# Kernel optimization log

Hardware: AMD Instinct MI355X
Metric: run time of the kernel (lower is better)

## Reference

```python
import jax, jax.numpy as jnp
import numpy as np
from math import factorial, sqrt, pi

# ---- sizes ----
LMAX = 2; K = 32; NL = 4; NB = 8; PPOLY = 5.0; RMAX = 10.0
N = 1000; E = 8000; G = 4; XDIM = 26; MLP = 128
LS = (0, 1, 2)

# ---- real Clebsch-Gordan couplings (Racah formula + complex->real basis change) ----
def _cg_c(j1, m1, j2, m2, J, M):
    if M != m1 + m2 or J < abs(j1 - j2) or J > j1 + j2:
        return 0.0
    f = factorial
    pre = sqrt((2*J+1) * f(J+j1-j2) * f(J-j1+j2) * f(j1+j2-J) / f(j1+j2+J+1))
    pre *= sqrt(f(J+M)*f(J-M)*f(j1-m1)*f(j1+m1)*f(j2-m2)*f(j2+m2))
    s = 0.0
    for k in range(j1 + j2 - J + 1):
        d = (k, j1+j2-J-k, j1-m1-k, j2+m2-k, J-j2+m1+k, J-j1-m2+k)
        if min(d) < 0:
            continue
        den = 1.0
        for t in d:
            den *= f(t)
        s += (-1.0)**k / den
    return pre * s

def _u(l):
    U = np.zeros((2*l+1, 2*l+1), dtype=complex)
    for m in range(-l, l+1):
        i = m + l
        if m < 0:
            U[i, m+l] = 1j/sqrt(2); U[i, -m+l] = -1j*((-1.0)**m)/sqrt(2)
        elif m == 0:
            U[i, l] = 1.0
        else:
            U[i, -m+l] = 1/sqrt(2); U[i, m+l] = ((-1.0)**m)/sqrt(2)
    return U

def _real_cg(l1, l2, l3):
    Tc = np.zeros((2*l1+1, 2*l2+1, 2*l3+1), dtype=complex)
    for m1 in range(-l1, l1+1):
        for m2 in range(-l2, l2+1):
            Tc[m1+l1, m2+l2, :] = [_cg_c(l1, m1, l2, m2, l3, m3) for m3 in range(-l3, l3+1)]
    T = np.einsum('am,bn,co,mno->abc', _u(l1), _u(l2), _u(l3).conj(), Tc)
    T = T.real if np.abs(T.real).sum() >= np.abs(T.imag).sum() else T.imag
    return jnp.asarray(np.ascontiguousarray(T), dtype=jnp.float32)

CG = {}
for _l1 in LS:
    for _l2 in LS:
        for _l3 in LS:
            if abs(_l1-_l2) <= _l3 <= _l1+_l2 and (_l1+_l2+_l3) % 2 == 0:
                CG[(_l1, _l2, _l3)] = _real_cg(_l1, _l2, _l3)

CONVH = sorted(CG.keys())                 # 11 parity-allowed (l_in, l_sh, l_out) paths
CONV0 = [p for p in CONVH if p[0] == 0]   # 3 paths for first layer (Kx0e input)
NUMEL0 = len(CONV0) * K * K
NUMELH = len(CONVH) * K * K

PAIRS = {lo: [(l1, l2) for l1 in LS for l2 in LS if (l1, l2, lo) in CG] for lo in LS}
TRIPLES = {lo: [(l1, l2, L, l3) for L in LS for l3 in LS if (L, l3, lo) in CG
                for (l1, l2) in PAIRS[L]] for lo in LS}
MAXP2 = max(len(PAIRS[lo]) for lo in LS)     # 4
MAXP3 = max(len(TRIPLES[lo]) for lo in LS)   # 15
CG3 = {}
for _lo in LS:
    for (_a, _b, _L, _c) in TRIPLES[_lo]:
        CG3[(_a, _b, _L, _c, _lo)] = jnp.einsum('ijl,lmo->ijmo', CG[(_a, _b, _L)], CG[(_L, _c, _lo)])

# ---- geometry embeddings ----
def _sph(u):  # u: [E,3] unit vectors; component-normalized real SH, l=0..2
    x, y, z = u[:, 0], u[:, 1], u[:, 2]
    y0 = jnp.ones_like(x)[:, None]
    y1 = sqrt(3.0) * jnp.stack([y, z, x], -1)
    y2 = jnp.stack([sqrt(15.0)*x*y, sqrt(15.0)*y*z, sqrt(5.0)/2*(3*z*z - 1),
                    sqrt(15.0)*x*z, sqrt(15.0)/2*(x*x - y*y)], -1)
    return (y0, y1, y2)

def _radial(r):  # r: [E,1] -> [E,NB] Bessel basis * polynomial cutoff (p=5)
    n = jnp.arange(1, NB + 1, dtype=r.dtype)
    bess = sqrt(2.0 / RMAX) * jnp.sin(n * pi * r / RMAX) / r
    u = r / RMAX
    p = PPOLY
    cut = 1 - (p+1)*(p+2)/2 * u**5 + p*(p+2) * u**6 - p*(p+1)/2 * u**7
    return bess * jnp.where(u < 1.0, cut, 0.0)

# ---- tensor-product conv: per-edge MLP weights -> gather, CG tensor product, scatter-sum ----
def _conv(h, src, dst, sh, ef, w1, b1, w2, b2, paths):
    w = jax.nn.relu(ef @ w1 + b1) @ w2 + b2          # [E, weight_numel]
    nto = {lo: max(1, sum(1 for q in paths if q[2] == lo)) for lo in LS}
    msg = [jnp.zeros((src.shape[0], K, 2*lo + 1), w.dtype) for lo in LS]
    off = 0
    for (li, ls, lo) in paths:
        wp = w[:, off:off + K*K].reshape(-1, K, K); off += K * K
        t = jnp.einsum('eui,es,iso->euo', h[li][src], sh[ls], CG[(li, ls, lo)])
        msg[lo] = msg[lo] + jnp.einsum('euo,euv->evo', t, wp) / sqrt(K * nto[lo])
    return [jnp.zeros((N, K, 2*lo + 1), w.dtype).at[dst].add(msg[lo]) for lo in LS]

def _bn(h, w, b, eps=1e-5):  # e3nn-style irreps batch norm (training stats)
    out = []
    for l in LS:
        xl = h[l]
        if l == 0:
            mu = jnp.mean(xl, axis=0, keepdims=True)
            var = jnp.mean((xl - mu)**2, axis=0, keepdims=True)
            out.append((xl - mu) / jnp.sqrt(var + eps) * w[l][None, :, None] + b[None, :, None])
        else:
            n2 = jnp.mean(jnp.sum(xl * xl, -1), axis=0)  # [K]
            out.append(xl / jnp.sqrt(n2 + eps)[None, :, None] * w[l][None, :, None])
    return out

# ---- equivariant product-basis block (per-channel symmetric contractions, correlation 3) ----
def _prod(A, sc, w1, w2, w3, wlin, target_ls, use_sc):
    out = []
    for lo in target_ls:
        acc = w1[lo][None, :, None] * A[lo]
        for p, (l1, l2) in enumerate(PAIRS[lo]):
            t = jnp.einsum('nki,nkj,ijo->nko', A[l1], A[l2], CG[(l1, l2, lo)])
            acc = acc + w2[lo, p][None, :, None] * t
        for p, (l1, l2, L, l3) in enumerate(TRIPLES[lo]):
            t = jnp.einsum('nki,nkj,nkm,ijmo->nko', A[l1], A[l2], A[l3], CG3[(l1, l2, L, l3, lo)])
            acc = acc + w3[lo, p][None, :, None] * t
        y = jnp.einsum('nki,kv->nvi', acc, wlin[lo])
        if use_sc:
            y = y + sc[lo]
        out.append(y)
    return out

def _forward(x, pos, w_emb, b_emb, fc0_w1, fc0_b1, fc0_w2, fc0_b2,
             fcs_w1, fcs_b1, fcs_w2, fcs_b2, bn_w, bn_b, pw1, pw2, pw3, plin,
             edge_index, batch):
    src, dst = edge_index[0], edge_index[1]
    vec = pos[src] - pos[dst]
    r = jnp.maximum(jnp.linalg.norm(vec, axis=-1, keepdims=True), 1e-6)
    sh = _sph(vec / r)
    ef = _radial(r)
    h0 = x @ w_emb + b_emb
    h = [h0[:, :, None], jnp.zeros((N, K, 3), h0.dtype), jnp.zeros((N, K, 5), h0.dtype)]
    for i in range(NL):
        if i == 0:
            m = _conv(h, src, dst, sh, ef, fc0_w1, fc0_b1, fc0_w2, fc0_b2, CONV0)
        else:
            j = i - 1
            m = _conv(h, src, dst, sh, ef, fcs_w1[j], fcs_b1[j], fcs_w2[j], fcs_b2[j], CONVH)
        m = _bn(m, bn_w[i], bn_b[i])
        last = (i == NL - 1)
        h = _prod(m, h, pw1[i], pw2[i], pw3[i], plin[i],
                  target_ls=((0,) if last else LS), use_sc=(not last))
    node = h[0][:, :, 0]                                  # [N, K]
    graph = jax.ops.segment_sum(node, batch, num_segments=G)
    return node, graph

def setup_inputs() -> dict:
    key = jax.random.key(0)
    ks = jax.random.split(key, 16)
    rn = lambda k, sh, s: jax.random.normal(k, sh, dtype=jnp.float32) * s
    return dict(
        x=rn(ks[0], (N, XDIM), 1.0),
        pos=rn(ks[1], (N, 3), 3.0),
        edge_index=jax.random.randint(ks[2], (2, E), 0, N, dtype=jnp.int32),
        batch=jnp.sort(jax.random.randint(ks[3], (N,), 0, G, dtype=jnp.int32)),
        w_emb=rn(ks[4], (XDIM, K), 1.0/sqrt(XDIM)), b_emb=jnp.zeros((K,), jnp.float32),
        fc0_w1=rn(ks[5], (NB, MLP), 1.0/sqrt(NB)), fc0_b1=jnp.zeros((MLP,), jnp.float32),
        fc0_w2=rn(ks[6], (MLP, NUMEL0), 1.0/sqrt(MLP)), fc0_b2=jnp.zeros((NUMEL0,), jnp.float32),
        fcs_w1=rn(ks[7], (NL-1, NB, MLP), 1.0/sqrt(NB)), fcs_b1=jnp.zeros((NL-1, MLP), jnp.float32),
        fcs_w2=rn(ks[8], (NL-1, MLP, NUMELH), 1.0/sqrt(MLP)), fcs_b2=jnp.zeros((NL-1, NUMELH), jnp.float32),
        bn_w=jnp.ones((NL, 3, K), jnp.float32), bn_b=jnp.zeros((NL, K), jnp.float32),
        pw1=rn(ks[9], (NL, 3, K), 0.5),
        pw2=rn(ks[10], (NL, 3, MAXP2, K), 0.3),
        pw3=rn(ks[11], (NL, 3, MAXP3, K), 0.1),
        plin=rn(ks[12], (NL, 3, K, K), 1.0/sqrt(K)),
    )

def reference(x, pos, edge_index, batch, w_emb, b_emb, fc0_w1, fc0_b1, fc0_w2, fc0_b2,
              fcs_w1, fcs_b1, fcs_w2, fcs_b2, bn_w, bn_b, pw1, pw2, pw3, plin):
    return _forward(x, pos, w_emb, b_emb, fc0_w1, fc0_b1, fc0_w2, fc0_b2,
                    fcs_w1, fcs_b1, fcs_w2, fcs_b2, bn_w, bn_b, pw1, pw2, pw3, plin,
                    edge_index, batch)
```

## Files before the change

kernel.cpp:

```cpp
#include <hip/hip_runtime.h>
#include <hip/hip_bf16.h>
#include <math.h>

#define NE 8000
#define NN 1000
#define CAP 64
#define PLANE 256000

typedef unsigned short ushortt;
typedef __attribute__((ext_vector_type(8))) short short8;
typedef __attribute__((ext_vector_type(4))) float f32x4;

__device__ const int KEYL[11][3] = {{0,0,0},{0,1,1},{0,2,2},{1,0,1},{1,1,0},{1,1,2},{1,2,1},{2,0,2},{2,1,1},{2,2,0},{2,2,2}};
__device__ const int KEYOFF[12] = {0,1,10,35,44,53,98,143,168,213,238,363};

struct PathT { int li, ls, lo, cgoff, comp; };
__device__ const PathT PATHS[11] = {
 {0,0,0,  0, 0},{0,1,1,  1, 1},{0,2,2, 10, 4},{1,0,1, 35, 9},{1,1,0, 44,12},{1,1,2, 53,13},
 {1,2,1, 98,18},{2,0,2,143,21},{2,1,1,168,26},{2,2,0,213,29},{2,2,2,238,30}};

struct CPair { int l1,l2,cga; };
struct CTrip { int l1,l2,L,cga,l3,cgb; };
constexpr CPair cPR0[3]={{0,0,0},{1,1,44},{2,2,213}};
constexpr CPair cPR1[4]={{0,1,1},{1,0,35},{1,2,98},{2,1,168}};
constexpr CPair cPR2[4]={{0,2,10},{1,1,53},{2,0,143},{2,2,238}};
constexpr CTrip cTR0[11]={
  {0,0,0,0,0,0},{1,1,0,44,0,0},{2,2,0,213,0,0},
  {0,1,1,1,1,44},{1,0,1,35,1,44},{1,2,1,98,1,44},{2,1,1,168,1,44},
  {0,2,2,10,2,213},{1,1,2,53,2,213},{2,0,2,143,2,213},{2,2,2,238,2,213}};
constexpr CTrip cTR1[15]={
  {0,0,0,0,1,1},{1,1,0,44,1,1},{2,2,0,213,1,1},
  {0,1,1,1,0,35},{1,0,1,35,0,35},{1,2,1,98,0,35},{2,1,1,168,0,35},
  {0,1,1,1,2,98},{1,0,1,35,2,98},{1,2,1,98,2,98},{2,1,1,168,2,98},
  {0,2,2,10,1,168},{1,1,2,53,1,168},{2,0,2,143,1,168},{2,2,2,238,1,168}};
constexpr CTrip cTR2[15]={
  {0,0,0,0,2,10},{1,1,0,44,2,10},{2,2,0,213,2,10},
  {0,1,1,1,1,53},{1,0,1,35,1,53},{1,2,1,98,1,53},{2,1,1,168,1,53},
  {0,2,2,10,0,143},{1,1,2,53,0,143},{2,0,2,143,0,143},{2,2,2,238,0,143},
  {0,2,2,10,2,238},{1,1,2,53,2,238},{2,0,2,143,2,238},{2,2,2,238,2,238}};
constexpr CPair getPR(int lo,int p){ return lo==0?cPR0[p]:(lo==1?cPR1[p]:cPR2[p]); }
constexpr CTrip getTR(int lo,int p){ return lo==0?cTR0[p]:(lo==1?cTR1[p]:cTR2[p]); }
constexpr int cloff(int l){ return l==0?0:(l==1?1:4); }
constexpr int nPR(int lo){ return lo==0?3:4; }
constexpr int nTR(int lo){ return lo==0?11:15; }

template<int I> struct ic_t { static constexpr int v = I; };
template<int N, int I=0, typename F>
__device__ __forceinline__ void sfor(F&& f){
  if constexpr (I < N){ f(ic_t<I>{}); sfor<N, I+1>((F&&)f); }
}

__device__ __forceinline__ int loff_(int l){ return l==0?0:(l==1?1:4); }

__device__ __forceinline__ ushortt f2bf(float x){
  union { float f; unsigned int u; } a; a.f = x;
  unsigned int r = a.u + 0x7FFFu + ((a.u >> 16) & 1u);
  return (ushortt)(r >> 16);
}

__device__ __forceinline__ void gload_lds16(const void* g, void* lds){
  __builtin_amdgcn_global_load_lds((const __attribute__((address_space(1))) void*)g,
                                   (__attribute__((address_space(3))) void*)lds, 16, 0, 0);
}

__device__ double d_fact(int n){ double f=1.0; for(int i=2;i<=n;i++) f*=(double)i; return f; }

__device__ double d_cg(int j1,int m1,int j2,int m2,int J,int M){
  if (M != m1+m2 || J < abs(j1-j2) || J > j1+j2) return 0.0;
  double pre = sqrt((2.0*J+1.0)*d_fact(J+j1-j2)*d_fact(J-j1+j2)*d_fact(j1+j2-J)/d_fact(j1+j2+J+1));
  pre *= sqrt(d_fact(J+M)*d_fact(J-M)*d_fact(j1-m1)*d_fact(j1+m1)*d_fact(j2-m2)*d_fact(j2+m2));
  double s=0.0;
  for(int k=0;k<=j1+j2-J;k++){
    int d0=k, d1=j1+j2-J-k, d2=j1-m1-k, d3=j2+m2-k, d4=J-j2+m1+k, d5=J-j1-m2+k;
    if (d0<0||d1<0||d2<0||d3<0||d4<0||d5<0) continue;
    double den = d_fact(d0)*d_fact(d1)*d_fact(d2)*d_fact(d3)*d_fact(d4)*d_fact(d5);
    s += ((k&1)?-1.0:1.0)/den;
  }
  return pre*s;
}

__device__ void d_u(int l, int i, int j, double* re, double* im){
  int m = i - l;
  *re=0.0; *im=0.0;
  const double s2 = 0.70710678118654752440;
  double par = (m & 1) ? -1.0 : 1.0;
  if (m < 0){
    if (j == m + l)  *im += s2;
    if (j == -m + l) *im += -par*s2;
  } else if (m == 0){
    if (j == l) *re = 1.0;
  } else {
    if (j == -m + l) *re += s2;
    if (j == m + l)  *re += par*s2;
  }
}

__global__ __launch_bounds__(128) void kcg1(double* tmp){
  int key = blockIdx.x;
  int l1=KEYL[key][0], l2=KEYL[key][1], l3=KEYL[key][2];
  int n1=2*l1+1, n2=2*l2+1, n3=2*l3+1;
  int nel=n1*n2*n3;
  int t=threadIdx.x;
  if (t>=nel) return;
  int a=t/(n2*n3), b=(t/n3)%n2, c=t%n3;
  double sre=0.0, sim=0.0;
  for (int mi=0;mi<n1;mi++)
    for (int ni=0;ni<n2;ni++){
      int m3 = (mi-l1)+(ni-l2);
      int oi = m3 + l3;
      if (oi<0 || oi>=n3) continue;
      double tc = d_cg(l1,mi-l1,l2,ni-l2,l3,m3);
      if (tc==0.0) continue;
      double r1,i1,r2,i2,r3,i3;
      d_u(l1,a,mi,&r1,&i1);
      d_u(l2,b,ni,&r2,&i2);
      d_u(l3,c,oi,&r3,&i3);
      double rr = r1*r2 - i1*i2;
      double ri = r1*i2 + i1*r2;
      double fr = rr*r3 + ri*i3;
      double fi = ri*r3 - rr*i3;
      sre += fr*tc; sim += fi*tc;
    }
  tmp[(size_t)(KEYOFF[key]+t)*2]   = sre;
  tmp[(size_t)(KEYOFF[key]+t)*2+1] = sim;
}

__global__ __launch_bounds__(64) void kcg2(const double* tmp, float* cgf){
  int key=threadIdx.x;
  if (key>=11) return;
  int off=KEYOFF[key], n=KEYOFF[key+1]-off;
  double sre=0.0, sim=0.0;
  for (int i=0;i<n;i++){ sre += fabs(tmp[(size_t)(off+i)*2]); sim += fabs(tmp[(size_t)(off+i)*2+1]); }
  bool takeRe = (sre >= sim);
  for (int i=0;i<n;i++) cgf[off+i] = (float)(takeRe ? tmp[(size_t)(off+i)*2] : tmp[(size_t)(off+i)*2+1]);
}

__global__ __launch_bounds__(256) void kgeom(const float* __restrict__ pos, const int* __restrict__ ei,
                                             float* __restrict__ shb, float* __restrict__ efb){
  int e = blockIdx.x*256+threadIdx.x;
  if (e>=NE) return;
  int s=ei[e], d=ei[NE+e];
  float vx=pos[s*3]-pos[d*3], vy=pos[s*3+1]-pos[d*3+1], vz=pos[s*3+2]-pos[d*3+2];
  float r = sqrtf(vx*vx+vy*vy+vz*vz);
  r = fmaxf(r, 1e-6f);
  float inv = 1.0f/r;
  float x=vx*inv, y=vy*inv, z=vz*inv;
  float* sh = shb + (size_t)e*9;
  const float s3=1.7320508075688772f, s15=3.872983346207417f, s5h=1.118033988749895f, s15h=1.9364916731037085f;
  sh[0]=1.0f;
  sh[1]=s3*y; sh[2]=s3*z; sh[3]=s3*x;
  sh[4]=s15*x*y; sh[5]=s15*y*z; sh[6]=s5h*(3.0f*z*z-1.0f); sh[7]=s15*x*z; sh[8]=s15h*(x*x-y*y);
  float u=r*0.1f;
  float cut=0.0f;
  if (u<1.0f){ float u2=u*u; float u5=u2*u2*u; cut = 1.0f - 21.0f*u5 + 35.0f*u5*u - 15.0f*u5*u2; }
  const float c0 = 0.4472135954999579f;
  const float PIF = 3.14159265358979323846f;
  float* ef = efb + (size_t)e*8;
  for (int j=0;j<8;j++)
    ef[j] = c0*sinf((float)(j+1)*PIF*r*0.1f)*inv*cut;
}

__global__ __launch_bounds__(256) void kembed(const float* __restrict__ x, const float* __restrict__ wemb,
                                              const float* __restrict__ bemb, float* __restrict__ h){
  int idx = blockIdx.x*256+threadIdx.x;
  if (idx>=NN*32) return;
  int n=idx>>5, k=idx&31;
  float a=bemb[k];
  for (int d=0;d<26;d++) a += x[n*26+d]*wemb[d*32+k];
  float* hp = h + (size_t)n*288 + k*9;
  hp[0]=a;
  #pragma unroll
  for (int c=1;c<9;c++) hp[c]=0.0f;
}

__global__ __launch_bounds__(256) void ktrans(const float* __restrict__ fc0_w2, const float* __restrict__ fcs_w2,
                                              ushortt* __restrict__ w2t0, ushortt* __restrict__ w2tH){
  int layer = blockIdx.z;
  int numel = (layer==0) ? 3072 : 11264;
  int c0 = blockIdx.x*32;
  if (c0 >= numel) return;
  const float* src = (layer==0) ? fc0_w2 : fcs_w2 + (size_t)(layer-1)*128*11264;
  ushortt* dst = (layer==0) ? w2t0 : w2tH + (size_t)(layer-1)*11264*128;
  int k0 = blockIdx.y*32;
  __shared__ float tile[32][33];
  int t = threadIdx.x;
  #pragma unroll
  for (int it=0; it<4; it++){
    int r = (t>>5) + it*8;
    tile[r][t&31] = src[(size_t)(k0+r)*numel + c0 + (t&31)];
  }
  __syncthreads();
  #pragma unroll
  for (int it=0; it<4; it++){
    int c = (t>>5) + it*8;
    int k = t&31;
    dst[(size_t)(c0+c)*128 + k0 + k] = f2bf(tile[k][c]);
  }
}

__global__ __launch_bounds__(256) void khid(const float* __restrict__ efb, const float* __restrict__ w1,
                                            const float* __restrict__ b1, ushortt* __restrict__ hidbf){
  int idx = blockIdx.x*256+threadIdx.x;
  if (idx >= NE*128) return;
  int e = idx>>7, m = idx&127;
  float a = b1[m];
  const float* ef = efb + (size_t)e*8;
  #pragma unroll
  for (int j=0;j<8;j++) a = fmaf(ef[j], w1[j*128+m], a);
  a = a>0.0f?a:0.0f;
  hidbf[idx] = f2bf(a);
}

template<int NO>
__global__ __launch_bounds__(256, (NO==1?3:2)) void kmsg5(
    const float* __restrict__ hc, const float* __restrict__ shb,
    const ushortt* __restrict__ hidbf, const ushortt* __restrict__ w2t,
    const float* __restrict__ b2, const float* __restrict__ cg,
    const int* __restrict__ src, float* __restrict__ msgp, int plist){
  int p = (plist >> (blockIdx.y*8)) & 0xFF;
  int e0 = blockIdx.x*64;
  int li=PATHS[p].li, ls=PATHS[p].ls;
  int n1=2*li+1, ns=2*ls+1;
  int lioff=loff_(li), lsoff=loff_(ls);
  int cgoff=PATHS[p].cgoff;
  int comp=PATHS[p].comp;

  __shared__ __align__(16) ushortt sB[2][64*128];
  __shared__ __align__(16) float   sT[NO*2048];
  __shared__ __align__(16) float   sB2[1024];
  __shared__ int     sSRC[64];
  float* ov  = (float*)&sB[1][0];
  float* sCP = ov;
  float* sSH = ov + 1600;

  int t = threadIdx.x;
  int w = t>>6, l = t&63;

  #pragma unroll
  for (int q=0;q<4;q++){
    int R0 = w*16 + q*4;
    int row = R0 + (l>>4);
    int ks = ((l&15)*8) ^ ((row&7)<<3);
    gload_lds16(w2t + (size_t)(p*1024 + row)*128 + ks, &sB[0][R0*128]);
  }
  short8 av[4];
  {
    const ushortt* ap = hidbf + (size_t)(e0 + w*16 + (l&15))*128 + (l>>4)*8;
    #pragma unroll
    for (int kk=0;kk<4;kk++) av[kk] = *(const short8*)(ap + kk*32);
  }
  #pragma unroll
  for (int q=0;q<4;q++) sB2[t + q*256] = b2[p*1024 + t + q*256];
  if (t < 64) sSRC[t] = src[e0+t];
  for (int idx=t; idx<64*9; idx+=256) sSH[idx] = shb[(size_t)e0*9 + idx];
  __syncthreads();

  for (int idx=t; idx<64*n1*NO; idx+=256){
    int e=idx/(n1*NO), r=idx%(n1*NO), i=r/NO, o=r%NO;
    float a=0.0f;
    for (int s=0;s<ns;s++) a += cg[cgoff + (i*ns+s)*NO+o]*sSH[e*9 + lsoff + s];
    sCP[e*25 + i*NO + o]=a;
  }
  __syncthreads();

  for (int idx=t; idx<64*32; idx+=256){
    int e = idx&63, u = idx>>6;
    const float* hp = hc + (size_t)sSRC[e]*288 + u*9 + lioff;
    float hv[5];
    #pragma unroll
    for (int i=0;i<5;i++) hv[i] = hp[i];
    #pragma unroll
    for (int o=0;o<NO;o++){
      float a=0.0f;
      #pragma unroll
      for (int i=0;i<5;i++) if (i<n1) a = fmaf(hv[i], sCP[e*25 + i*NO + o], a);
      sT[(u*NO+o)*64 + e] = a;
    }
  }
  __syncthreads();

  float macc[4][2][NO];
  #pragma unroll
  for (int r=0;r<4;r++)
    #pragma unroll
    for (int vh=0;vh<2;vh++)
      #pragma unroll
      for (int o=0;o<NO;o++) macc[r][vh][o]=0.0f;

  int e_idx = w*16 + (l>>4)*4;

  for (int c=0;c<16;c++){
    int buf = c&1;
    if (c<15){
      #pragma unroll
      for (int q=0;q<4;q++){
        int R0 = w*16 + q*4;
        int row = R0 + (l>>4);
        int ks = ((l&15)*8) ^ ((row&7)<<3);
        gload_lds16(w2t + (size_t)(p*1024 + (c+1)*64 + row)*128 + ks, &sB[buf^1][R0*128]);
      }
    }
    f32x4 acc[4];
    #pragma unroll
    for (int fn=0;fn<4;fn++)
      #pragma unroll
      for (int r=0;r<4;r++) acc[fn][r]=0.0f;
    __builtin_amdgcn_s_setprio(1);
    #pragma unroll
    for (int kk=0; kk<4; kk++){
      #pragma unroll
      for (int fn=0; fn<4; fn++){
        int brow = fn*16 + (l&15);
        int kb = (kk*32 + (l>>4)*8) ^ ((brow&7)<<3);
        short8 bv = *(const short8*)&sB[buf][brow*128 + kb];
        acc[fn] = __builtin_amdgcn_mfma_f32_16x16x32_bf16(av[kk], bv, acc[fn], 0,0,0);
      }
    }
    __builtin_amdgcn_s_setprio(0);
    #pragma unroll
    for (int uu=0;uu<2;uu++){
      int ug = c*2 + uu;
      f32x4 tv[NO];
      #pragma unroll
      for (int o=0;o<NO;o++) tv[o] = *(const f32x4*)&sT[(ug*NO+o)*64 + e_idx];
      #pragma unroll
      for (int vh=0;vh<2;vh++){
        int fn = uu*2+vh;
        float b2v = sB2[c*64 + fn*16 + (l&15)];
        #pragma unroll
        for (int r=0;r<4;r++){
          float Cv = acc[fn][r] + b2v;
          #pragma unroll
          for (int o=0;o<NO;o++) macc[r][vh][o] = fmaf(Cv, tv[o][r], macc[r][vh][o]);
        }
      }
    }
    __syncthreads();
  }

  float* sW = sT;
  #pragma unroll
  for (int r=0;r<4;r++){
    int e = e_idx + r;
    #pragma unroll
    for (int vh=0;vh<2;vh++){
      int v = vh*16 + (l&15);
      int g = v>>2;
      int addr = e*32 + (((g ^ (e&7)))<<2) + (v&3);
      #pragma unroll
      for (int o=0;o<NO;o++)
        sW[o*2048 + addr] = macc[r][vh][o];
    }
  }
  __syncthreads();
  for (int j=t; j<NO*512; j+=256){
    int o = j>>9, q = j&511;
    int e = q>>3, gl = q&7;
    f32x4 vv = *(const f32x4*)&sW[o*2048 + e*32 + ((gl^(e&7))<<2)];
    *(f32x4*)(msgp + (size_t)(comp+o)*PLANE + (size_t)e0*32 + q*4) = vv;
  }
}

__global__ __launch_bounds__(320) void kbuild(const int* __restrict__ dst, int* __restrict__ cnt, int* __restrict__ lst){
  int n = blockIdx.x;
  int t = threadIdx.x;
  __shared__ int s_dstl[NE];
  __shared__ int s_cnt[321];
  for (int idx=t; idx<NE; idx+=320) s_dstl[idx]=dst[idx];
  __syncthreads();
  const int per = NE/320;
  int start=t*per, end=start+per;
  int c=0;
  for (int e=start;e<end;++e) if (s_dstl[e]==n) c++;
  s_cnt[t+1]=c;
  if (t==0) s_cnt[0]=0;
  __syncthreads();
  if (t==0){ for (int i=1;i<=320;i++) s_cnt[i]+=s_cnt[i-1]; }
  __syncthreads();
  int pos = s_cnt[t];
  for (int e=start;e<end;++e) if (s_dstl[e]==n){ if (pos<CAP) lst[n*CAP+pos]=e; pos++; }
  if (t==0){ int M=s_cnt[320]; cnt[n]=(M<CAP)?M:CAP; }
}

__global__ __launch_bounds__(320) void kgather2(const float* __restrict__ msgp, const int* __restrict__ cnt,
                                                const int* __restrict__ lst, float* __restrict__ mbuf, int full){
  int n = blockIdx.x;
  int t = threadIdx.x;
  if (t >= 288) return;
  int M = cnt[n];
  int jc = t>>5, k = t&31;
  float acc=0.0f;
  if (full){
    int pl0,pl1,pl2,pl3,np;
    if (jc==0){ pl0=0; pl1=12; pl2=29; pl3=0; np=3; }
    else if (jc<4){ int o=jc-1; pl0=1+o; pl1=9+o; pl2=18+o; pl3=26+o; np=4; }
    else { int o=jc-4; pl0=4+o; pl1=13+o; pl2=21+o; pl3=30+o; np=4; }
    for (int m=0;m<M;++m){
      int e = lst[n*CAP+m];
      int base = e*32 + k;
      float a = msgp[(size_t)pl0*PLANE + base] + msgp[(size_t)pl1*PLANE + base] + msgp[(size_t)pl2*PLANE + base];
      if (np==4) a += msgp[(size_t)pl3*PLANE + base];
      acc += a;
    }
  } else {
    for (int m=0;m<M;++m){
      int e = lst[n*CAP+m];
      acc += msgp[(size_t)jc*PLANE + e*32 + k];
    }
  }
  float norm = full ? (jc==0 ? 0.10206207261596577f : 0.08838834764831845f) : 0.17677669529663687f;
  mbuf[(size_t)n*288 + k*9 + jc] = acc*norm;
}

__global__ __launch_bounds__(256) void kbn(const float* __restrict__ mbuf, float* __restrict__ stats){
  int k = blockIdx.x, t = threadIdx.x;
  float s0=0,sq0=0,sq1=0,sq2=0;
  for (int n=t;n<NN;n+=256){
    const float* mp = mbuf + (size_t)n*288 + k*9;
    float v0=mp[0]; s0+=v0; sq0+=v0*v0;
    float a=mp[1],b=mp[2],c=mp[3]; sq1+=a*a+b*b+c*c;
    float d=mp[4],e=mp[5],f=mp[6],g=mp[7],h=mp[8]; sq2+=d*d+e*e+f*f+g*g+h*h;
  }
  __shared__ float r[4][256];
  r[0][t]=s0; r[1][t]=sq0; r[2][t]=sq1; r[3][t]=sq2;
  __syncthreads();
  for (int s=128;s>0;s>>=1){
    if (t<s){ r[0][t]+=r[0][t+s]; r[1][t]+=r[1][t+s]; r[2][t]+=r[2][t+s]; r[3][t]+=r[3][t+s]; }
    __syncthreads();
  }
  if (t==0){
    float mu = r[0][0]/(float)NN;
    float var = r[1][0]/(float)NN - mu*mu;
    stats[k]      = mu;
    stats[32+k]   = rsqrtf(var + 1e-5f);
    stats[64+k]   = rsqrtf(r[2][0]/(float)NN + 1e-5f);
    stats[96+k]   = rsqrtf(r[3][0]/(float)NN + 1e-5f);
  }
}

template<int CGA,int NA,int AO,int NB,int BO,int NO>
__device__ __forceinline__ void c2u(const float* __restrict__ cg, const float (&A)[9], const float (&B)[9], float (&out)[5]){
  #pragma unroll
  for (int o=0;o<NO;o++) out[o]=0.0f;
  #pragma unroll
  for (int i=0;i<NA;i++){
    #pragma unroll
    for (int j=0;j<NB;j++){
      float ab=A[AO+i]*B[BO+j];
      #pragma unroll
      for (int o=0;o<NO;o++) out[o]=fmaf(ab, cg[CGA+(i*NB+j)*NO+o], out[o]);
    }
  }
}
template<int CGA,int NA,int NB,int BO,int NO>
__device__ __forceinline__ void c2u5(const float* __restrict__ cg, const float (&Bb)[5], const float (&A)[9], float (&out)[5]){
  #pragma unroll
  for (int o=0;o<NO;o++) out[o]=0.0f;
  #pragma unroll
  for (int i=0;i<NA;i++){
    #pragma unroll
    for (int j=0;j<NB;j++){
      float ab=Bb[i]*A[BO+j];
      #pragma unroll
      for (int o=0;o<NO;o++) out[o]=fmaf(ab, cg[CGA+(i*NB+j)*NO+o], out[o]);
    }
  }
}

template<int LO>
__device__ __forceinline__ void do_lo(const float* __restrict__ cg, const float (&A)[9], float (&L)[9],
                                      const float* __restrict__ w1, const float* __restrict__ w2,
                                      const float* __restrict__ w3, int k){
  constexpr int NO=2*LO+1, AO=cloff(LO);
  float acc[5];
  float wc = w1[LO*32+k];
  #pragma unroll
  for (int o=0;o<NO;o++) acc[o]=wc*A[AO+o];
  sfor<nPR(LO)>([&](auto pc){
    constexpr int p = decltype(pc)::v;
    constexpr CPair P = getPR(LO,p);
    float tt[5];
    c2u<P.cga, 2*P.l1+1, cloff(P.l1), 2*P.l2+1, cloff(P.l2), NO>(cg, A, A, tt);
    float w = w2[(LO*4+p)*32+k];
    #pragma unroll
    for (int o=0;o<NO;o++) acc[o]=fmaf(w, tt[o], acc[o]);
  });
  sfor<nTR(LO)>([&](auto pc){
    constexpr int p = decltype(pc)::v;
    constexpr CTrip T = getTR(LO,p);
    constexpr int NL=2*T.L+1;
    float bb[5];
    c2u<T.cga, 2*T.l1+1, cloff(T.l1), 2*T.l2+1, cloff(T.l2), NL>(cg, A, A, bb);
    float tt[5];
    c2u5<T.cgb, NL, 2*T.l3+1, cloff(T.l3), NO>(cg, bb, A, tt);
    float w = w3[(LO*15+p)*32+k];
    #pragma unroll
    for (int o=0;o<NO;o++) acc[o]=fmaf(w, tt[o], acc[o]);
  });
  #pragma unroll
  for (int o=0;o<NO;o++) L[AO+o]=acc[o];
}

template<int LAST>
__global__ __launch_bounds__(256) void kprod3(const float* __restrict__ mbuf, const float* __restrict__ stats,
    const float* __restrict__ hc, float* __restrict__ hn,
    const float* __restrict__ bnw, const float* __restrict__ bnb,
    const float* __restrict__ w1, const float* __restrict__ w2, const float* __restrict__ w3,
    const float* __restrict__ plin, const float* __restrict__ cg, float* __restrict__ nodeout){
  int t = threadIdx.x;
  int nl = t>>5, k = t&31;
  int n = blockIdx.x*8 + nl;
  __shared__ float sL[8][32][9];
  float A[9], L[9];
  #pragma unroll
  for (int j=0;j<9;j++) L[j]=0.0f;
  const float* mp = mbuf + (size_t)n*288 + k*9;
  {
    float a0 = (mp[0]-stats[k])*stats[32+k]*bnw[k] + bnb[k];
    float f1 = stats[64+k]*bnw[32+k];
    float f2 = stats[96+k]*bnw[64+k];
    A[0]=a0;
    A[1]=mp[1]*f1; A[2]=mp[2]*f1; A[3]=mp[3]*f1;
    #pragma unroll
    for (int c=0;c<5;c++) A[4+c]=mp[4+c]*f2;
  }
  do_lo<0>(cg, A, L, w1, w2, w3, k);
  if constexpr (!LAST){
    do_lo<1>(cg, A, L, w1, w2, w3, k);
    do_lo<2>(cg, A, L, w1, w2, w3, k);
  }
  #pragma unroll
  for (int j=0;j<9;j++) sL[nl][k][j]=L[j];
  __syncthreads();

  if constexpr (!LAST){
    for (int idx=t; idx<8*288; idx+=256){
      int n2 = idx/288;
      int r  = idx%288;
      int jc = r>>5, v = r&31;
      int lo = (jc==0)?0:((jc<4)?1:2);
      float y=0.0f;
      const float* pl = plin + lo*1024 + v;
      for (int kk=0;kk<32;kk++)
        y = fmaf(sL[n2][kk][jc], pl[kk*32], y);
      int ng = blockIdx.x*8 + n2;
      y += hc[(size_t)ng*288 + v*9 + jc];
      hn[(size_t)ng*288 + v*9 + jc] = y;
    }
  } else {
    int n2 = t>>5, v = t&31;
    float y=0.0f;
    const float* pl = plin + v;
    for (int kk=0;kk<32;kk++)
      y = fmaf(sL[n2][kk][0], pl[kk*32], y);
    nodeout[(size_t)(blockIdx.x*8+n2)*32 + v] = y;
  }
}

__global__ __launch_bounds__(256) void kgraphA(const float* __restrict__ nodeout, const int* __restrict__ batch,
                                               float* __restrict__ partial){
  int b = blockIdx.x;
  int t = threadIdx.x;
  __shared__ float sv[8][32];
  __shared__ int   sg[8];
  int nl = t>>5, k = t&31;
  int n = b*8 + nl;
  sv[nl][k] = nodeout[(size_t)n*32 + k];
  if (k==0) sg[nl] = batch[n];
  __syncthreads();
  if (t < 128){
    int g = t>>5, kk = t&31;
    float acc=0.0f;
    #pragma unroll
    for (int j=0;j<8;j++) if (sg[j]==g) acc += sv[j][kk];
    partial[((size_t)b*4 + g)*32 + kk] = acc;
  }
}

__global__ __launch_bounds__(128) void kgraphB(const float* __restrict__ partial, float* __restrict__ gout){
  int t = threadIdx.x;
  int g = t>>5, k = t&31;
  float acc=0.0f;
  for (int b=0;b<125;b++) acc += partial[((size_t)b*4 + g)*32 + k];
  gout[g*32 + k] = acc;
}

extern "C" void kernel_launch(void* const* d_in, const int* in_sizes, int n_in,
                              void* d_out, int out_size, void* d_ws, size_t ws_size,
                              hipStream_t stream) {
  const float* x      = (const float*)d_in[0];
  const float* pos    = (const float*)d_in[1];
  const int*   ei     = (const int*)d_in[2];
  const int*   batch  = (const int*)d_in[3];
  const float* w_emb  = (const float*)d_in[4];
  const float* b_emb  = (const float*)d_in[5];
  const float* fc0_w1 = (const float*)d_in[6];
  const float* fc0_b1 = (const float*)d_in[7];
  const float* fc0_w2 = (const float*)d_in[8];
  const float* fc0_b2 = (const float*)d_in[9];
  const float* fcs_w1 = (const float*)d_in[10];
  const float* fcs_b1 = (const float*)d_in[11];
  const float* fcs_w2 = (const float*)d_in[12];
  const float* fcs_b2 = (const float*)d_in[13];
  const float* bn_w   = (const float*)d_in[14];
  const float* bn_b   = (const float*)d_in[15];
  const float* pw1    = (const float*)d_in[16];
  const float* pw2    = (const float*)d_in[17];
  const float* pw3    = (const float*)d_in[18];
  const float* plin   = (const float*)d_in[19];

  double* cgtmp = (double*)d_ws;
  float*  F     = (float*)d_ws;
  float*  cgf   = F + 1456;
  float*  shb   = F + 1824;
  float*  efb   = F + 73824;
  float*  hA    = F + 137824;
  float*  hB    = F + 425824;
  float*  mbuf  = F + 713824;
  float*  stats = F + 1001824;
  float*  msgb  = F + 1001952;
  ushortt* hidbf = (ushortt*)(F + 9961952);
  ushortt* w2t0  = (ushortt*)(F + 10473952);
  ushortt* w2tH  = (ushortt*)(F + 10670560);
  int* csr_cnt = (int*)(F + 12833248);
  int* csr_lst = csr_cnt + 1024;
  float* partial = F + 12900000;

  float* nodeout = (float*)d_out;
  float* gout    = (float*)d_out + NN*32;

  kcg1<<<11,128,0,stream>>>(cgtmp);
  kcg2<<<1,64,0,stream>>>(cgtmp, cgf);
  kgeom<<<(NE+255)/256,256,0,stream>>>(pos, ei, shb, efb);
  kembed<<<(NN*32+255)/256,256,0,stream>>>(x, w_emb, b_emb, hA);
  ktrans<<<dim3(352,4,4),256,0,stream>>>(fc0_w2, fcs_w2, w2t0, w2tH);
  kbuild<<<NN,320,0,stream>>>(ei+NE, csr_cnt, csr_lst);

  float* hc = hA;
  float* hn = hB;
  for (int i=0;i<4;i++){
    const float *w1,*b1,*b2; const ushortt* w2t; int full;
    if (i==0){ w1=fc0_w1; b1=fc0_b1; w2t=w2t0; b2=fc0_b2; full=0; }
    else {
      int j=i-1;
      w1=fcs_w1 + (size_t)j*1024;
      b1=fcs_b1 + (size_t)j*128;
      w2t=w2tH + (size_t)j*11264*128;
      b2=fcs_b2 + (size_t)j*11264;
      full=1;
    }
    khid<<<(NE*128+255)/256,256,0,stream>>>(efb, w1, b1, hidbf);
    if (full){
      kmsg5<1><<<dim3(125,3),256,0,stream>>>(hc, shb, hidbf, w2t, b2, cgf, ei, msgb, 0 | (4<<8) | (9<<16));
      kmsg5<3><<<dim3(125,4),256,0,stream>>>(hc, shb, hidbf, w2t, b2, cgf, ei, msgb, 1 | (3<<8) | (6<<16) | (8<<24));
      kmsg5<5><<<dim3(125,4),256,0,stream>>>(hc, shb, hidbf, w2t, b2, cgf, ei, msgb, 2 | (5<<8) | (7<<16) | (10<<24));
    } else {
      kmsg5<1><<<dim3(125,1),256,0,stream>>>(hc, shb, hidbf, w2t, b2, cgf, ei, msgb, 0);
      kmsg5<3><<<dim3(125,1),256,0,stream>>>(hc, shb, hidbf, w2t, b2, cgf, ei, msgb, 1);
      kmsg5<5><<<dim3(125,1),256,0,stream>>>(hc, shb, hidbf, w2t, b2, cgf, ei, msgb, 2);
    }
    kgather2<<<NN,320,0,stream>>>(msgb, csr_cnt, csr_lst, mbuf, full);
    kbn<<<32,256,0,stream>>>(mbuf, stats);
    int last = (i==3);
    const float* bw = bn_w + (size_t)i*96;
    const float* bb = bn_b + (size_t)i*32;
    const float* p1 = pw1 + (size_t)i*96;
    const float* p2 = pw2 + (size_t)i*384;
    const float* p3 = pw3 + (size_t)i*1440;
    const float* pl = plin + (size_t)i*3072;
    if (!last)
      kprod3<0><<<NN/8,256,0,stream>>>(mbuf, stats, hc, hn, bw, bb, p1, p2, p3, pl, cgf, nodeout);
    else
      kprod3<1><<<NN/8,256,0,stream>>>(mbuf, stats, hc, hn, bw, bb, p1, p2, p3, pl, cgf, nodeout);
    float* tmp=hc; hc=hn; hn=tmp;
  }
  kgraphA<<<125,256,0,stream>>>(nodeout, batch, partial);
  kgraphB<<<1,128,0,stream>>>(partial, gout);
}
```

Measured before the change: 586.7 us.

## Load MFMA B-operand weights directly from global into registers, drop LDS staging

The message kernel no longer stages the per-path MLP output weights (w2t) through a double-buffered LDS tile via async global-to-LDS loads. Each wave now reads its B fragments straight from global memory into registers every chunk, and also reads the bias from global. This removes the per-chunk barrier and shrinks LDS use, which should allow more resident blocks. The cost is that all four waves read the same weight rows redundantly, the prefetch overlap is lost, and the loads are exposed just before each MFMA sequence.

```diff
diff --git a/kernel.cpp b/kernel.cpp
--- a/kernel.cpp
+++ b/kernel.cpp
@@ -56,11 +56,6 @@
   union { float f; unsigned int u; } a; a.f = x;
   unsigned int r = a.u + 0x7FFFu + ((a.u >> 16) & 1u);
   return (ushortt)(r >> 16);
-}
-
-__device__ __forceinline__ void gload_lds16(const void* g, void* lds){
-  __builtin_amdgcn_global_load_lds((const __attribute__((address_space(1))) void*)g,
-                                   (__attribute__((address_space(3))) void*)lds, 16, 0, 0);
 }
 
 __device__ double d_fact(int n){ double f=1.0; for(int i=2;i<=n;i++) f*=(double)i; return f; }
@@ -212,7 +207,7 @@
 }
 
 template<int NO>
-__global__ __launch_bounds__(256, (NO==1?3:2)) void kmsg5(
+__global__ __launch_bounds__(256, 2) void kmsg6(
     const float* __restrict__ hc, const float* __restrict__ shb,
     const ushortt* __restrict__ hidbf, const ushortt* __restrict__ w2t,
     const float* __restrict__ b2, const float* __restrict__ cg,
@@ -225,32 +220,20 @@
   int cgoff=PATHS[p].cgoff;
   int comp=PATHS[p].comp;
 
-  __shared__ __align__(16) ushortt sB[2][64*128];
-  __shared__ __align__(16) float   sT[NO*2048];
-  __shared__ __align__(16) float   sB2[1024];
-  __shared__ int     sSRC[64];
-  float* ov  = (float*)&sB[1][0];
-  float* sCP = ov;
-  float* sSH = ov + 1600;
+  __shared__ __align__(16) float sT[NO*2048];
+  __shared__ __align__(16) float sCP[64*25];
+  __shared__ __align__(16) float sSH[64*9];
+  __shared__ int sSRC[64];
 
   int t = threadIdx.x;
   int w = t>>6, l = t&63;
 
-  #pragma unroll
-  for (int q=0;q<4;q++){
-    int R0 = w*16 + q*4;
-    int row = R0 + (l>>4);
-    int ks = ((l&15)*8) ^ ((row&7)<<3);
-    gload_lds16(w2t + (size_t)(p*1024 + row)*128 + ks, &sB[0][R0*128]);
-  }
   short8 av[4];
   {
     const ushortt* ap = hidbf + (size_t)(e0 + w*16 + (l&15))*128 + (l>>4)*8;
     #pragma unroll
     for (int kk=0;kk<4;kk++) av[kk] = *(const short8*)(ap + kk*32);
   }
-  #pragma unroll
-  for (int q=0;q<4;q++) sB2[t + q*256] = b2[p*1024 + t + q*256];
   if (t < 64) sSRC[t] = src[e0+t];
   for (int idx=t; idx<64*9; idx+=256) sSH[idx] = shb[(size_t)e0*9 + idx];
   __syncthreads();
@@ -288,17 +271,16 @@
       for (int o=0;o<NO;o++) macc[r][vh][o]=0.0f;
 
   int e_idx = w*16 + (l>>4)*4;
+  const ushortt* bbase = w2t + (size_t)(p*1024 + (l&15))*128 + (l>>4)*8;
+  const float*   b2base = b2 + p*1024 + (l&15);
 
   for (int c=0;c<16;c++){
-    int buf = c&1;
-    if (c<15){
-      #pragma unroll
-      for (int q=0;q<4;q++){
-        int R0 = w*16 + q*4;
-        int row = R0 + (l>>4);
-        int ks = ((l&15)*8) ^ ((row&7)<<3);
-        gload_lds16(w2t + (size_t)(p*1024 + (c+1)*64 + row)*128 + ks, &sB[buf^1][R0*128]);
-      }
+    short8 bb[4][4];
+    #pragma unroll
+    for (int fn=0;fn<4;fn++){
+      const ushortt* bp = bbase + (size_t)(c*64 + fn*16)*128;
+      #pragma unroll
+      for (int kk=0;kk<4;kk++) bb[fn][kk] = *(const short8*)(bp + kk*32);
     }
     f32x4 acc[4];
     #pragma unroll
@@ -307,15 +289,10 @@
       for (int r=0;r<4;r++) acc[fn][r]=0.0f;
     __builtin_amdgcn_s_setprio(1);
     #pragma unroll
-    for (int kk=0; kk<4; kk++){
-      #pragma unroll
-      for (int fn=0; fn<4; fn++){
-        int brow = fn*16 + (l&15);
-        int kb = (kk*32 + (l>>4)*8) ^ ((brow&7)<<3);
-        short8 bv = *(const short8*)&sB[buf][brow*128 + kb];
-        acc[fn] = __builtin_amdgcn_mfma_f32_16x16x32_bf16(av[kk], bv, acc[fn], 0,0,0);
-      }
-    }
+    for (int kk=0; kk<4; kk++)
+      #pragma unroll
+      for (int fn=0; fn<4; fn++)
+        acc[fn] = __builtin_amdgcn_mfma_f32_16x16x32_bf16(av[kk], bb[fn][kk], acc[fn], 0,0,0);
     __builtin_amdgcn_s_setprio(0);
     #pragma unroll
     for (int uu=0;uu<2;uu++){
@@ -326,7 +303,7 @@
       #pragma unroll
       for (int vh=0;vh<2;vh++){
         int fn = uu*2+vh;
-        float b2v = sB2[c*64 + fn*16 + (l&15)];
+        float b2v = b2base[c*64 + fn*16];
         #pragma unroll
         for (int r=0;r<4;r++){
           float Cv = acc[fn][r] + b2v;
@@ -335,8 +312,8 @@
         }
       }
     }
-    __syncthreads();
-  }
+  }
+  __syncthreads();
 
   float* sW = sT;
   #pragma unroll
@@ -651,13 +628,13 @@
     }
     khid<<<(NE*128+255)/256,256,0,stream>>>(efb, w1, b1, hidbf);
     if (full){
-      kmsg5<1><<<dim3(125,3),256,0,stream>>>(hc, shb, hidbf, w2t, b2, cgf, ei, msgb, 0 | (4<<8) | (9<<16));
-      kmsg5<3><<<dim3(125,4),256,0,stream>>>(hc, shb, hidbf, w2t, b2, cgf, ei, msgb, 1 | (3<<8) | (6<<16) | (8<<24));
-      kmsg5<5><<<dim3(125,4),256,0,stream>>>(hc, shb, hidbf, w2t, b2, cgf, ei, msgb, 2 | (5<<8) | (7<<16) | (10<<24));
+      kmsg6<1><<<dim3(125,3),256,0,stream>>>(hc, shb, hidbf, w2t, b2, cgf, ei, msgb, 0 | (4<<8) | (9<<16));
+      kmsg6<3><<<dim3(125,4),256,0,stream>>>(hc, shb, hidbf, w2t, b2, cgf, ei, msgb, 1 | (3<<8) | (6<<16) | (8<<24));
+      kmsg6<5><<<dim3(125,4),256,0,stream>>>(hc, shb, hidbf, w2t, b2, cgf, ei, msgb, 2 | (5<<8) | (7<<16) | (10<<24));
     } else {
-      kmsg5<1><<<dim3(125,1),256,0,stream>>>(hc, shb, hidbf, w2t, b2, cgf, ei, msgb, 0);
-      kmsg5<3><<<dim3(125,1),256,0,stream>>>(hc, shb, hidbf, w2t, b2, cgf, ei, msgb, 1);
-      kmsg5<5><<<dim3(125,1),256,0,stream>>>(hc, shb, hidbf, w2t, b2, cgf, ei, msgb, 2);
+      kmsg6<1><<<dim3(125,1),256,0,stream>>>(hc, shb, hidbf, w2t, b2, cgf, ei, msgb, 0);
+      kmsg6<3><<<dim3(125,1),256,0,stream>>>(hc, shb, hidbf, w2t, b2, cgf, ei, msgb, 1);
+      kmsg6<5><<<dim3(125,1),256,0,stream>>>(hc, shb, hidbf, w2t, b2, cgf, ei, msgb, 2);
     }
     kgather2<<<NN,320,0,stream>>>(msgb, csr_cnt, csr_lst, mbuf, full);
     kbn<<<32,256,0,stream>>>(mbuf, stats);
```

New measurement: 996.7 us. +69.9%, slower.
